# Performance work log

Hardware: AMD Instinct MI355X
Metric: run time of the kernel (lower is better)

Reference implementation:

```python
import jax, jax.numpy as jnp
import numpy as np

N, D = 8192, 256


def setup_inputs() -> dict:
    key = jax.random.key(0)
    ka, kb = jax.random.split(key)
    latent_a = jax.random.normal(ka, (N, D), dtype=jnp.float32)
    latent_b = jax.random.normal(kb, (N, D), dtype=jnp.float32)
    return {"latent_a": latent_a, "latent_b": latent_b}


def _rbf_kernel(x, y):
    # kernel[i,j] = exp(-mean_d((x_i - y_j)^2) / D) = exp(-||x_i - y_j||^2 / D^2)
    d = x.shape[1]
    sq = (
        jnp.sum(x * x, axis=1)[:, None]
        + jnp.sum(y * y, axis=1)[None, :]
        - 2.0 * (x @ y.T)
    )  # [Nx, Ny] squared distances (no O(N^2 D) intermediate)
    return jnp.exp(-sq / (d * d))


def reference(latent_a, latent_b):
    x = latent_a.reshape(latent_a.shape[0], -1)
    y = latent_b.reshape(latent_b.shape[0], -1)
    x_kernel = _rbf_kernel(x, x)
    y_kernel = _rbf_kernel(y, y)
    xy_kernel = _rbf_kernel(x, y)
    return jnp.mean(x_kernel) + jnp.mean(y_kernel) - 2.0 * jnp.mean(xy_kernel)
```

## Files before the change

### kernel.cpp

```cpp
#include <hip/hip_runtime.h>
#include <math.h>


#define NPTS  8192
#define DIM   256
#define MTOT  (2 * NPTS)
#define TILE  128
#define BK    64
#define NTILE (MTOT / TILE)
#define XTILE (NPTS / TILE)
#define NTRI  (NTILE * (NTILE + 1) / 2)

typedef short bf16x8 __attribute__((ext_vector_type(8)));
typedef float f32x4  __attribute__((ext_vector_type(4)));

#define GLDS(g, l)                                                          \
    __builtin_amdgcn_global_load_lds(                                       \
        (const __attribute__((address_space(1))) void*)(g),                 \
        (__attribute__((address_space(3))) void*)(l), 16, 0, 0)

__device__ __forceinline__ uint rn_bf16(float x) {
    uint u = __float_as_uint(x);
    return (u + 0x7FFFu + ((u >> 16) & 1u)) >> 16;
}

__global__ __launch_bounds__(256) void mmd_prep(const float* __restrict__ a,
                                                const float* __restrict__ b,
                                                ushort* __restrict__ zh,
                                                float* __restrict__ norms) {
    const int row  = blockIdx.x * 4 + (threadIdx.x >> 6);
    const int lane = threadIdx.x & 63;
    const float* src = (row < NPTS) ? (a + (size_t)row * DIM)
                                    : (b + (size_t)(row - NPTS) * DIM);
    float4 v = *reinterpret_cast<const float4*>(src + lane * 4);
    float s = v.x * v.x + v.y * v.y + v.z * v.z + v.w * v.w;

    uint2 packed = make_uint2(rn_bf16(v.x) | (rn_bf16(v.y) << 16),
                              rn_bf16(v.z) | (rn_bf16(v.w) << 16));
    *reinterpret_cast<uint2*>(&zh[(size_t)row * DIM + lane * 4]) = packed;

    #pragma unroll
    for (int off = 32; off > 0; off >>= 1) s += __shfl_down(s, off);
    if (lane == 0) norms[row] = s;
}

__device__ __forceinline__ void unrank(int p, int& I, int& J) {
    I = (int)(NTILE + 0.5 - sqrt((NTILE + 0.5) * (NTILE + 0.5) - 2.0 * p));
    int base = I * NTILE - I * (I - 1) / 2;
    if (p < base)                     { --I; base = I * NTILE - I * (I - 1) / 2; }
    else if (p >= base + (NTILE - I)) { ++I; base = I * NTILE - I * (I - 1) / 2; }
    J = I + (p - base);
}

__global__ __launch_bounds__(256, 3) void mmd_gram(const ushort* __restrict__ zh,
                                                   const float* __restrict__ norms,
                                                   double* __restrict__ partials) {
    int I, J;
    unrank(blockIdx.x, I, J);

    __shared__ ushort sI[TILE * BK];
    __shared__ ushort sJ[TILE * BK];
    __shared__ double wsum[4];

    const int t   = threadIdx.x;
    const int l   = t & 63;
    const int wid = t >> 6;
    const int wy  = (wid >> 1) * 64;
    const int wx  = (wid & 1) * 64;

    const int    rbase = (wid & 1) * 64;
    const ushort* gtile = zh + (size_t)(((wid < 2) ? I : J) * TILE) * DIM;
    ushort*       ltile = (wid < 2) ? sI : sJ;
    const int lrow = l >> 3;
    const int gch  = (l & 7) ^ lrow;
    const ushort* gsrc = gtile + (size_t)(rbase + lrow) * DIM + gch * 8;
    ushort*       ldst = ltile + (size_t)(rbase) * BK + (size_t)l * 8;

    f32x4 acc[4][4];
    #pragma unroll
    for (int bi = 0; bi < 4; ++bi)
        #pragma unroll
        for (int bj = 0; bj < 4; ++bj)
            acc[bi][bj] = (f32x4)0.0f;

    const int ar = l & 15;
    const int cc = l >> 4;
    const int sw = ar & 7;

    for (int k0 = 0; k0 < DIM; k0 += BK) {
        __syncthreads();
        #pragma unroll
        for (int g = 0; g < 8; ++g)
            GLDS(gsrc + (size_t)g * 8 * DIM + k0, ldst + (size_t)g * 8 * BK);
        __syncthreads();

        #pragma unroll
        for (int s = 0; s < 2; ++s) {
            bf16x8 aF[4];
            #pragma unroll
            for (int bi = 0; bi < 4; ++bi) {
                const int rI = wy + bi * 16 + ar;
                const int ch = (s * 4 + cc) ^ sw;
                aF[bi] = *reinterpret_cast<const bf16x8*>(&sI[rI * BK + ch * 8]);
            }
            #pragma unroll
            for (int bj = 0; bj < 4; ++bj) {
                const int rJ = wx + bj * 16 + ar;
                const int ch = (s * 4 + cc) ^ sw;
                bf16x8 bF = *reinterpret_cast<const bf16x8*>(&sJ[rJ * BK + ch * 8]);
                #pragma unroll
                for (int bi = 0; bi < 4; ++bi)
                    acc[bi][bj] = __builtin_amdgcn_mfma_f32_16x16x32_bf16(
                                      aF[bi], bF, acc[bi][bj], 0, 0, 0);
            }
        }
    }

    const int rg = (l >> 4) * 4;
    double tsum = 0.0;
    #pragma unroll
    for (int bi = 0; bi < 4; ++bi) {
        float ni[4];
        #pragma unroll
        for (int r = 0; r < 4; ++r)
            ni[r] = norms[I * TILE + wy + bi * 16 + rg + r];
        #pragma unroll
        for (int bj = 0; bj < 4; ++bj) {
            const float nj = norms[J * TILE + wx + bj * 16 + (l & 15)];
            #pragma unroll
            for (int r = 0; r < 4; ++r) {
                float sq = ni[r] + nj - 2.0f * acc[bi][bj][r];
                tsum += (double)__expf(sq * (-1.0f / 65536.0f));
            }
        }
    }

    const double sgn  = ((I < XTILE) == (J < XTILE)) ? 1.0 : -1.0;
    const double mult = (I == J) ? sgn : 2.0 * sgn;
    tsum *= mult;

    #pragma unroll
    for (int off = 32; off > 0; off >>= 1) tsum += __shfl_down(tsum, off);
    if (l == 0) wsum[wid] = tsum;
    __syncthreads();
    if (t == 0) partials[blockIdx.x] = wsum[0] + wsum[1] + wsum[2] + wsum[3];
}

__global__ __launch_bounds__(256) void mmd_reduce(const double* __restrict__ partials,
                                                  float* __restrict__ out) {
    double s = 0.0;
    for (int i = threadIdx.x; i < NTRI; i += 256) s += partials[i];
    #pragma unroll
    for (int off = 32; off > 0; off >>= 1) s += __shfl_down(s, off);
    __shared__ double wsum[4];
    const int wid = threadIdx.x >> 6, lane = threadIdx.x & 63;
    if (lane == 0) wsum[wid] = s;
    __syncthreads();
    if (threadIdx.x == 0)
        out[0] = (float)((wsum[0] + wsum[1] + wsum[2] + wsum[3]) /
                         ((double)NPTS * (double)NPTS));
}

extern "C" void kernel_launch(void* const* d_in, const int* in_sizes, int n_in,
                              void* d_out, int out_size, void* d_ws, size_t ws_size,
                              hipStream_t stream) {
    const float* a = (const float*)d_in[0];
    const float* b = (const float*)d_in[1];
    float* out = (float*)d_out;

    const size_t zElems = (size_t)MTOT * DIM;
    ushort* zh    = (ushort*)d_ws;
    float*  norms = (float*)(zh + zElems);
    double* partials = (double*)(norms + MTOT);

    mmd_prep<<<MTOT / 4, 256, 0, stream>>>(a, b, zh, norms);
    mmd_gram<<<NTRI, 256, 0, stream>>>(zh, norms, partials);
    mmd_reduce<<<1, 256, 0, stream>>>(partials, out);
}
```

Baseline: 158.4 us.

## Double-buffer LDS tiles, use exp2 with prescaled norms, remap blocks across XCDs

Unrolls the K loop into a double-buffered schedule so the next LDS stage load overlaps the MFMA work on the current one. Norms are prescaled by -log2(e)/D^2 in the prep kernel so the epilogue does one fma plus exp2, with per-row float accumulation replacing per-element double adds. Block indices are permuted across the eight XCD groups, and launch bounds drop to 2 blocks per CU to accommodate the doubled LDS footprint. The float accumulation slightly reduces precision, and occupancy falls.

```diff
diff --git a/kernel.cpp b/kernel.cpp
--- a/kernel.cpp
+++ b/kernel.cpp
@@ -14,6 +14,9 @@
 typedef short bf16x8 __attribute__((ext_vector_type(8)));
 typedef float f32x4  __attribute__((ext_vector_type(4)));
 
+#define C2F   4.4027101e-5f
+#define NSCF  (-2.20135502845565e-5f)
+
 #define GLDS(g, l)                                                          \
     __builtin_amdgcn_global_load_lds(                                       \
         (const __attribute__((address_space(1))) void*)(g),                 \
@@ -27,7 +30,7 @@
 __global__ __launch_bounds__(256) void mmd_prep(const float* __restrict__ a,
                                                 const float* __restrict__ b,
                                                 ushort* __restrict__ zh,
-                                                float* __restrict__ norms) {
+                                                float* __restrict__ nsc) {
     const int row  = blockIdx.x * 4 + (threadIdx.x >> 6);
     const int lane = threadIdx.x & 63;
     const float* src = (row < NPTS) ? (a + (size_t)row * DIM)
@@ -41,7 +44,7 @@
 
     #pragma unroll
     for (int off = 32; off > 0; off >>= 1) s += __shfl_down(s, off);
-    if (lane == 0) norms[row] = s;
+    if (lane == 0) nsc[row] = s * NSCF;
 }
 
 __device__ __forceinline__ void unrank(int p, int& I, int& J) {
@@ -52,14 +55,15 @@
     J = I + (p - base);
 }
 
-__global__ __launch_bounds__(256, 3) void mmd_gram(const ushort* __restrict__ zh,
-                                                   const float* __restrict__ norms,
+__global__ __launch_bounds__(256, 2) void mmd_gram(const ushort* __restrict__ zh,
+                                                   const float* __restrict__ nsc,
                                                    double* __restrict__ partials) {
+    const int p = (blockIdx.x & 7) * (NTRI / 8) + (blockIdx.x >> 3);
     int I, J;
-    unrank(blockIdx.x, I, J);
+    unrank(p, I, J);
 
-    __shared__ ushort sI[TILE * BK];
-    __shared__ ushort sJ[TILE * BK];
+    __shared__ ushort sI0[TILE * BK], sI1[TILE * BK];
+    __shared__ ushort sJ0[TILE * BK], sJ1[TILE * BK];
     __shared__ double wsum[4];
 
     const int t   = threadIdx.x;
@@ -68,13 +72,21 @@
     const int wy  = (wid >> 1) * 64;
     const int wx  = (wid & 1) * 64;
 
-    const int    rbase = (wid & 1) * 64;
+    const int     rbase = (wid & 1) * 64;
     const ushort* gtile = zh + (size_t)(((wid < 2) ? I : J) * TILE) * DIM;
-    ushort*       ltile = (wid < 2) ? sI : sJ;
-    const int lrow = l >> 3;
-    const int gch  = (l & 7) ^ lrow;
-    const ushort* gsrc = gtile + (size_t)(rbase + lrow) * DIM + gch * 8;
-    ushort*       ldst = ltile + (size_t)(rbase) * BK + (size_t)l * 8;
+    const int     lrow  = l >> 3;
+    const int     gch   = (l & 7) ^ lrow;
+    const ushort* gsrc  = gtile + (size_t)(rbase + lrow) * DIM + gch * 8;
+    const int     ldoff = rbase * BK + l * 8;
+
+#define STAGE(dI, dJ, k0)                                                   \
+    do {                                                                    \
+        ushort* ld = ((wid < 2) ? (dI) : (dJ)) + ldoff;                     \
+        const ushort* gs = gsrc + (k0);                                     \
+        _Pragma("unroll")                                                   \
+        for (int g = 0; g < 8; ++g)                                         \
+            GLDS(gs + (size_t)g * 8 * DIM, ld + g * 8 * BK);                \
+    } while (0)
 
     f32x4 acc[4][4];
     #pragma unroll
@@ -87,54 +99,62 @@
     const int cc = l >> 4;
     const int sw = ar & 7;
 
-    for (int k0 = 0; k0 < DIM; k0 += BK) {
-        __syncthreads();
-        #pragma unroll
-        for (int g = 0; g < 8; ++g)
-            GLDS(gsrc + (size_t)g * 8 * DIM + k0, ldst + (size_t)g * 8 * BK);
-        __syncthreads();
+#define COMPUTE(cI, cJ)                                                     \
+    do {                                                                    \
+        _Pragma("unroll")                                                   \
+        for (int s = 0; s < 2; ++s) {                                       \
+            bf16x8 aF[4];                                                   \
+            const int ch = (s * 4 + cc) ^ sw;                               \
+            _Pragma("unroll")                                               \
+            for (int bi = 0; bi < 4; ++bi)                                  \
+                aF[bi] = *reinterpret_cast<const bf16x8*>(                  \
+                             &(cI)[(wy + bi * 16 + ar) * BK + ch * 8]);     \
+            _Pragma("unroll")                                               \
+            for (int bj = 0; bj < 4; ++bj) {                                \
+                bf16x8 bF = *reinterpret_cast<const bf16x8*>(               \
+                             &(cJ)[(wx + bj * 16 + ar) * BK + ch * 8]);     \
+                _Pragma("unroll")                                           \
+                for (int bi = 0; bi < 4; ++bi)                              \
+                    acc[bi][bj] = __builtin_amdgcn_mfma_f32_16x16x32_bf16(  \
+                                      aF[bi], bF, acc[bi][bj], 0, 0, 0);    \
+            }                                                               \
+        }                                                                   \
+    } while (0)
 
-        #pragma unroll
-        for (int s = 0; s < 2; ++s) {
-            bf16x8 aF[4];
-            #pragma unroll
-            for (int bi = 0; bi < 4; ++bi) {
-                const int rI = wy + bi * 16 + ar;
-                const int ch = (s * 4 + cc) ^ sw;
-                aF[bi] = *reinterpret_cast<const bf16x8*>(&sI[rI * BK + ch * 8]);
-            }
-            #pragma unroll
-            for (int bj = 0; bj < 4; ++bj) {
-                const int rJ = wx + bj * 16 + ar;
-                const int ch = (s * 4 + cc) ^ sw;
-                bf16x8 bF = *reinterpret_cast<const bf16x8*>(&sJ[rJ * BK + ch * 8]);
-                #pragma unroll
-                for (int bi = 0; bi < 4; ++bi)
-                    acc[bi][bj] = __builtin_amdgcn_mfma_f32_16x16x32_bf16(
-                                      aF[bi], bF, acc[bi][bj], 0, 0, 0);
-            }
-        }
-    }
+    STAGE(sI0, sJ0, 0);
+    __syncthreads();
+    STAGE(sI1, sJ1, BK);
+    COMPUTE(sI0, sJ0);
+    __syncthreads();
+    STAGE(sI0, sJ0, 2 * BK);
+    COMPUTE(sI1, sJ1);
+    __syncthreads();
+    STAGE(sI1, sJ1, 3 * BK);
+    COMPUTE(sI0, sJ0);
+    __syncthreads();
+    COMPUTE(sI1, sJ1);
 
     const int rg = (l >> 4) * 4;
-    double tsum = 0.0;
+    float racc0 = 0.f, racc1 = 0.f, racc2 = 0.f, racc3 = 0.f;
     #pragma unroll
     for (int bi = 0; bi < 4; ++bi) {
         float ni[4];
         #pragma unroll
         for (int r = 0; r < 4; ++r)
-            ni[r] = norms[I * TILE + wy + bi * 16 + rg + r];
+            ni[r] = nsc[I * TILE + wy + bi * 16 + rg + r];
+        float rs = 0.f;
         #pragma unroll
         for (int bj = 0; bj < 4; ++bj) {
-            const float nj = norms[J * TILE + wx + bj * 16 + (l & 15)];
+            const float nj = nsc[J * TILE + wx + bj * 16 + (l & 15)];
             #pragma unroll
-            for (int r = 0; r < 4; ++r) {
-                float sq = ni[r] + nj - 2.0f * acc[bi][bj][r];
-                tsum += (double)__expf(sq * (-1.0f / 65536.0f));
-            }
+            for (int r = 0; r < 4; ++r)
+                rs += exp2f(fmaf(acc[bi][bj][r], C2F, ni[r] + nj));
         }
+        if (bi == 0) racc0 = rs; else if (bi == 1) racc1 = rs;
+        else if (bi == 2) racc2 = rs; else racc3 = rs;
     }
 
+    double tsum = ((double)racc0 + racc1) + ((double)racc2 + racc3);
     const double sgn  = ((I < XTILE) == (J < XTILE)) ? 1.0 : -1.0;
     const double mult = (I == J) ? sgn : 2.0 * sgn;
     tsum *= mult;
@@ -143,7 +163,7 @@
     for (int off = 32; off > 0; off >>= 1) tsum += __shfl_down(tsum, off);
     if (l == 0) wsum[wid] = tsum;
     __syncthreads();
-    if (t == 0) partials[blockIdx.x] = wsum[0] + wsum[1] + wsum[2] + wsum[3];
+    if (t == 0) partials[p] = wsum[0] + wsum[1] + wsum[2] + wsum[3];
 }
 
 __global__ __launch_bounds__(256) void mmd_reduce(const double* __restrict__ partials,
@@ -170,10 +190,10 @@
 
     const size_t zElems = (size_t)MTOT * DIM;
     ushort* zh    = (ushort*)d_ws;
-    float*  norms = (float*)(zh + zElems);
-    double* partials = (double*)(norms + MTOT);
+    float*  nsc   = (float*)(zh + zElems);
+    double* partials = (double*)(nsc + MTOT);
 
-    mmd_prep<<<MTOT / 4, 256, 0, stream>>>(a, b, zh, norms);
-    mmd_gram<<<NTRI, 256, 0, stream>>>(zh, norms, partials);
+    mmd_prep<<<MTOT / 4, 256, 0, stream>>>(a, b, zh, nsc);
+    mmd_gram<<<NTRI, 256, 0, stream>>>(zh, nsc, partials);
     mmd_reduce<<<1, 256, 0, stream>>>(partials, out);
 }
```

After: 179.6 us. 1.13x slower.
